# Performance work log

Hardware: AMD Instinct MI355X
Metric: run time of the kernel (lower is better)

The kernel has to match this reference:

```python
import jax, jax.numpy as jnp
import numpy as np

B, T, C, HS = 4, 4096, 1024, 128

def setup_inputs() -> dict:
    key = jax.random.key(0)
    kx, kq, kk, kv = jax.random.split(key, 4)
    x = jax.random.normal(kx, (B, T, C), dtype=jnp.float32)
    # bias-free Linear weights, stored as (in, out) so projection is x @ W
    scale = 1.0 / np.sqrt(C)
    Wq = jax.random.normal(kq, (C, HS), dtype=jnp.float32) * scale
    Wk = jax.random.normal(kk, (C, HS), dtype=jnp.float32) * scale
    Wv = jax.random.normal(kv, (C, HS), dtype=jnp.float32) * scale
    return {"x": x, "Wq": Wq, "Wk": Wk, "Wv": Wv}

def reference(x, Wq, Wk, Wv):
    # x: (B,T,C) -> q,k,v: (B,T,HS)
    q = jnp.einsum('btc,ch->bth', x, Wq)
    k = jnp.einsum('btc,ch->bth', x, Wk)
    v = jnp.einsum('btc,ch->bth', x, Wv)
    hs = k.shape[-1]
    # scaled scores (B,T,T) with causal mask
    wei = jnp.einsum('bth,bsh->bts', q, k) * (hs ** -0.5)
    causal = jnp.tril(jnp.ones((q.shape[1], q.shape[1]), dtype=bool))
    wei = jnp.where(causal, wei, -jnp.inf)
    wei = jax.nn.softmax(wei, axis=-1)
    # dropout p=0.0 -> identity
    out = jnp.einsum('bts,bsh->bth', wei, v)
    return out
```

## Files before the change

### kernel.cpp

```cpp
#include <hip/hip_runtime.h>
#include <hip/hip_bf16.h>

typedef __attribute__((ext_vector_type(8))) short short8;
typedef __attribute__((ext_vector_type(4))) float f32x4;
typedef __attribute__((ext_vector_type(16))) float f32x16;

#define BATCH 4
#define TLEN 4096
#define CDIM 1024
#define HSD 128
#define MROWS (BATCH*TLEN)

#define QSCALE 0.12751744f

__device__ __forceinline__ unsigned short f2bf(float f){
    unsigned u = __builtin_bit_cast(unsigned, f);
    u = (u + 0x7FFFu + ((u >> 16) & 1u)) >> 16;
    return (unsigned short)u;
}
__device__ __forceinline__ unsigned pkbf(float a, float b){
    unsigned ua = (__builtin_bit_cast(unsigned, a) + 0x8000u) >> 16;
    unsigned ub = (__builtin_bit_cast(unsigned, b) + 0x8000u) & 0xFFFF0000u;
    return ua | ub;
}

__global__ void prep_w_k(const float* __restrict__ Wq, const float* __restrict__ Wk,
                         const float* __restrict__ Wv, unsigned short* __restrict__ Wt){
    __shared__ float tile[32][33];
    const int w = blockIdx.z;
    const float* W = (w == 0) ? Wq : ((w == 1) ? Wk : Wv);
    const int c0 = blockIdx.x * 32, h0 = blockIdx.y * 32;
    const int lx = threadIdx.x & 31, ly = threadIdx.x >> 5;
#pragma unroll
    for (int i = 0; i < 4; i++){
        int c = c0 + ly + i * 8;
        tile[ly + i * 8][lx] = W[(size_t)c * HSD + h0 + lx];
    }
    __syncthreads();
#pragma unroll
    for (int i = 0; i < 4; i++){
        int h = h0 + ly + i * 8;
        Wt[((size_t)w * HSD + h) * CDIM + c0 + lx] = f2bf(tile[lx][ly + i * 8]);
    }
}

__device__ __forceinline__ void stage_wb(unsigned short* buf, const unsigned short* g, int tid){
#pragma unroll
    for (int i = 0; i < 3; i++){
        int c = i * 512 + tid;
        int row = c >> 2, kp = c & 3;
        int swz = (row & 3) ^ ((row >> 2) & 3);
        const unsigned short* gp = g + (size_t)row * CDIM + ((kp ^ swz) << 3);
        unsigned short* lp = buf + (c << 3);
        __builtin_amdgcn_global_load_lds((const __attribute__((address_space(1))) void*)gp,
                                         (__attribute__((address_space(3))) void*)lp, 16, 0, 0);
    }
}

__global__ __launch_bounds__(512) void proj_k(const float* __restrict__ x,
                                              const unsigned short* __restrict__ Wt,
                                              unsigned short* __restrict__ Qb,
                                              unsigned short* __restrict__ Kb,
                                              unsigned short* __restrict__ Vt){
    __shared__ unsigned short As[2][64 * 32];
    __shared__ unsigned short Bs[2][384 * 32];

    const int tid = threadIdx.x, lane = tid & 63, wave = tid >> 6;
    const int m = lane & 15, quad = lane >> 4;
    const int wr = wave & 1;
    const int wc = wave >> 1;
    const int rb = blockIdx.x * 64;

    const float* gA = x + (size_t)rb * CDIM;

    const int arow = tid >> 3, ach = tid & 7;
    const int asw = (arow & 3) ^ ((arow >> 2) & 3);
    const float* agp = gA + (size_t)arow * CDIM + ((((ach >> 1) ^ asw) << 3) + (ach & 1) * 4);
    unsigned short* asp0 = &As[0][arow * 32 + (ach << 2)];
    unsigned short* asp1 = &As[1][arow * 32 + (ach << 2)];

    f32x4 acc[6][2];
#pragma unroll
    for (int i = 0; i < 6; i++)
#pragma unroll
        for (int j = 0; j < 2; j++) acc[i][j] = (f32x4)0.f;

    stage_wb(&Bs[0][0], Wt, tid);
    {
        float4 a0 = *(const float4*)(agp);
        ushort4 o;
        o.x = f2bf(a0.x); o.y = f2bf(a0.y); o.z = f2bf(a0.z); o.w = f2bf(a0.w);
        *(ushort4*)asp0 = o;
    }
    __syncthreads();

    int cur = 0;
    for (int kc = 0; kc < CDIM / 32; ++kc){
        float4 a0n;
        if (kc + 1 < CDIM / 32){
            a0n = *(const float4*)(agp + (kc + 1) * 32);
            stage_wb(&Bs[cur ^ 1][0], Wt + (kc + 1) * 32, tid);
            asm volatile("s_waitcnt vmcnt(4)" ::: "memory");
        } else {
            asm volatile("s_waitcnt vmcnt(0)" ::: "memory");
        }
        __builtin_amdgcn_s_barrier();
        __builtin_amdgcn_sched_barrier(0);
        {
            short8 aF[6], bF[2];
#pragma unroll
            for (int i = 0; i < 6; i++){
                int ra = wc * 96 + i * 16 + m;
                int sa = (ra & 3) ^ ((ra >> 2) & 3);
                aF[i] = *(const short8*)&Bs[cur][ra * 32 + ((quad ^ sa) << 3)];
            }
#pragma unroll
            for (int j = 0; j < 2; j++){
                int rn = wr * 32 + j * 16 + m;
                int sb = (rn & 3) ^ ((rn >> 2) & 3);
                bF[j] = *(const short8*)&As[cur][rn * 32 + ((quad ^ sb) << 3)];
            }
#pragma unroll
            for (int i = 0; i < 6; i++)
#pragma unroll
                for (int j = 0; j < 2; j++)
                    acc[i][j] = __builtin_amdgcn_mfma_f32_16x16x32_bf16(aF[i], bF[j], acc[i][j], 0, 0, 0);
        }
        if (kc + 1 < CDIM / 32){
            ushort4 o;
            o.x = f2bf(a0n.x); o.y = f2bf(a0n.y); o.z = f2bf(a0n.z); o.w = f2bf(a0n.w);
            *(ushort4*)((cur == 0) ? asp1 : asp0) = o;
        }
        cur ^= 1;
    }
    __builtin_amdgcn_s_barrier();

    const int b = rb >> 12;
#pragma unroll
    for (int i = 0; i < 6; i++){
        const int hbase = wc * 96 + i * 16;
        const int type = hbase >> 7;
        const int hp = hbase + quad * 4;
#pragma unroll
        for (int j = 0; j < 2; j++){
            const int t = rb + wr * 32 + j * 16 + m;
            if (type == 0){
                ushort4 v;
                v.x = f2bf(acc[i][j][0] * QSCALE); v.y = f2bf(acc[i][j][1] * QSCALE);
                v.z = f2bf(acc[i][j][2] * QSCALE); v.w = f2bf(acc[i][j][3] * QSCALE);
                *(ushort4*)(Qb + (size_t)t * HSD + hp) = v;
            } else if (type == 1){
                ushort4 v;
                v.x = f2bf(acc[i][j][0]); v.y = f2bf(acc[i][j][1]);
                v.z = f2bf(acc[i][j][2]); v.w = f2bf(acc[i][j][3]);
                *(ushort4*)(Kb + (size_t)t * HSD + (hp - 128)) = v;
            } else {
                const int tt = t & (TLEN - 1);
#pragma unroll
                for (int r = 0; r < 4; r++)
                    Vt[((size_t)b * HSD + (hp - 256 + r)) * TLEN + tt] = f2bf(acc[i][j][r]);
            }
        }
    }
}

__device__ __forceinline__ void stage_k_tile(unsigned short* buf, const unsigned short* g,
                                             int tid){
#pragma unroll
    for (int i = 0; i < 2; i++){
        int slot = i * 256 + tid;
        int row = slot >> 4;
        int ch  = slot & 15;
        const unsigned short* gp = g + row * 128 + ((ch ^ (row & 15)) << 3);
        unsigned short* lp = buf + (slot << 3);
        __builtin_amdgcn_global_load_lds((const __attribute__((address_space(1))) void*)gp,
                                         (__attribute__((address_space(3))) void*)lp, 16, 0, 0);
    }
}
__device__ __forceinline__ void stage_v_tile(unsigned short* buf, const unsigned short* g,
                                             int tid){
#pragma unroll
    for (int i = 0; i < 2; i++){
        int slot = i * 256 + tid;
        int row = slot >> 2;
        int ch  = slot & 3;
        const unsigned short* gp = g + (size_t)row * TLEN + ((ch ^ (row & 3)) << 3);
        unsigned short* lp = buf + (slot << 3);
        __builtin_amdgcn_global_load_lds((const __attribute__((address_space(1))) void*)gp,
                                         (__attribute__((address_space(3))) void*)lp, 16, 0, 0);
    }
}

__global__ __launch_bounds__(256, 3) void attn_k(const unsigned short* __restrict__ Qb,
                       const unsigned short* __restrict__ Kb,
                       const unsigned short* __restrict__ Vts,
                       float* __restrict__ Opart, float* __restrict__ lpart, int seglen){
    __shared__ unsigned short Kt[2][32 * 128];
    __shared__ unsigned short Vs[2][128 * 32];

    const int tid = threadIdx.x, lane = tid & 63, wave = tid >> 6;
    const int col = lane & 31, half = lane >> 5;
    const int q0 = ((int)gridDim.x - 1 - (int)blockIdx.x) * 128;
    const int seg = blockIdx.y, b = blockIdx.z;
    const int g0 = seg * seglen;
    if (g0 >= q0 + 128) return;
    const int gend = min(g0 + seglen, q0 + 128);
    const int nT = (gend - g0) >> 5;

    const int q0w = q0 + wave * 32;
    const size_t rowg = (size_t)b * TLEN + q0w;

    const unsigned short* kbase = Kb + (size_t)b * TLEN * HSD;
    const unsigned short* vbase = Vts + (size_t)b * HSD * TLEN;

    short8 aQ[8];
#pragma unroll
    for (int ks = 0; ks < 8; ks++)
        aQ[ks] = *(const short8*)(Qb + (rowg + col) * HSD + ks * 16 + half * 8);

    stage_k_tile(&Kt[0][0], kbase + (size_t)g0 * HSD, tid);
    stage_v_tile(&Vs[0][0], vbase + g0, tid);

    f32x16 accO[4];
#pragma unroll
    for (int i = 0; i < 4; i++) accO[i] = (f32x16)0.f;
    float lp = 0.f;

    asm volatile("s_waitcnt vmcnt(0)" ::: "memory");
#pragma unroll
    for (int ks = 0; ks < 8; ks++){
        f32x4 q_ = __builtin_bit_cast(f32x4, aQ[ks]);
        asm volatile("" : "+v"(q_));
        aQ[ks] = __builtin_bit_cast(short8, q_);
    }

    int cur = 0;
    for (int t = 0; t < nT; ++t){
        const int s0 = g0 + t * 32;
        if (t + 1 < nT){
            stage_k_tile(&Kt[cur ^ 1][0], kbase + (size_t)(s0 + 32) * HSD, tid);
            stage_v_tile(&Vs[cur ^ 1][0], vbase + (s0 + 32), tid);
            asm volatile("s_waitcnt vmcnt(4)" ::: "memory");
        } else {
            asm volatile("s_waitcnt vmcnt(0)" ::: "memory");
        }
        __builtin_amdgcn_s_barrier();
        __builtin_amdgcn_sched_barrier(0);
        if (s0 <= q0w + 31){
            const unsigned short* Ktc = &Kt[cur][0];
            const unsigned short* Vsc = &Vs[cur][0];
            f32x16 S = (f32x16)0.f;
            __builtin_amdgcn_s_setprio(1);
#pragma unroll
            for (int ks = 0; ks < 8; ks++){
                short8 aK = *(const short8*)&Ktc[col * 128 + (((ks * 2 + half) ^ (col & 15)) << 3)];
                S = __builtin_amdgcn_mfma_f32_32x32x16_bf16(aK, aQ[ks], S, 0, 0, 0);
            }
            __builtin_amdgcn_s_setprio(0);
            if (s0 + 31 > q0w){
                int qg = q0w + col;
#pragma unroll
                for (int r = 0; r < 16; r++){
                    int sg = s0 + (r & 3) + 8 * (r >> 2) + 4 * half;
                    if (sg > qg) S[r] = -1e30f;
                }
            }
            float p[16];
#pragma unroll
            for (int r = 0; r < 16; r++) p[r] = exp2f(S[r]);
#pragma unroll
            for (int r = 0; r < 16; r++) lp += p[r];
            short8 aP[2];
            {
                unsigned x1 = pkbf(p[0], p[1]), x2 = pkbf(p[2], p[3]);
                unsigned y1 = pkbf(p[4], p[5]), y2 = pkbf(p[6], p[7]);
                asm volatile("v_permlane32_swap_b32 %0, %1" : "+v"(x1), "+v"(y1));
                asm volatile("v_permlane32_swap_b32 %0, %1" : "+v"(x2), "+v"(y2));
                uint4 u; u.x = x1; u.y = x2; u.z = y1; u.w = y2;
                aP[0] = __builtin_bit_cast(short8, u);
                unsigned z1 = pkbf(p[8], p[9]),  z2 = pkbf(p[10], p[11]);
                unsigned w1 = pkbf(p[12], p[13]), w2 = pkbf(p[14], p[15]);
                asm volatile("v_permlane32_swap_b32 %0, %1" : "+v"(z1), "+v"(w1));
                asm volatile("v_permlane32_swap_b32 %0, %1" : "+v"(z2), "+v"(w2));
                uint4 u2; u2.x = z1; u2.y = z2; u2.z = w1; u2.w = w2;
                aP[1] = __builtin_bit_cast(short8, u2);
            }
            __builtin_amdgcn_s_setprio(1);
#pragma unroll
            for (int ks = 0; ks < 2; ks++){
#pragma unroll
                for (int ht = 0; ht < 4; ht++){
                    short8 bV = *(const short8*)&Vsc[(ht * 32 + col) * 32 +
                            (((ks * 2 + half) ^ (col & 3)) << 3)];
                    accO[ht] = __builtin_amdgcn_mfma_f32_32x32x16_bf16(aP[ks], bV, accO[ht], 0, 0, 0);
                }
            }
            __builtin_amdgcn_s_setprio(0);
        }
        __builtin_amdgcn_sched_barrier(0);
        __builtin_amdgcn_s_barrier();
        cur ^= 1;
    }
    lp += __shfl_xor(lp, 32, 64);
    if (lane < 32)
        lpart[(size_t)seg * MROWS + rowg + col] = lp;
    float* ob = Opart + (size_t)seg * MROWS * HSD;
#pragma unroll
    for (int ht = 0; ht < 4; ht++)
#pragma unroll
        for (int r = 0; r < 16; r++){
            int qrow = (r & 3) + 8 * (r >> 2) + 4 * half;
            ob[(rowg + qrow) * HSD + ht * 32 + col] = accO[ht][r];
        }
}

__global__ void merge_k(const float* __restrict__ Opart, const float* __restrict__ lpart,
                        float* __restrict__ out, int nseg, int seglen){
    int idx = blockIdx.x * 256 + threadIdx.x;
    int row = idx >> 7;
    int t = row & (TLEN - 1);
    int q0 = t & ~127;
    int nsv = min(nseg, (q0 + 127) / seglen + 1);
    float L = 0.f, o = 0.f;
    for (int s = 0; s < nsv; s++){
        L += lpart[(size_t)s * MROWS + row];
        o += Opart[(size_t)s * MROWS * HSD + idx];
    }
    out[idx] = o / L;
}

extern "C" void kernel_launch(void* const* d_in, const int* in_sizes, int n_in,
                              void* d_out, int out_size, void* d_ws, size_t ws_size,
                              hipStream_t stream) {
    const float* x  = (const float*)d_in[0];
    const float* Wq = (const float*)d_in[1];
    const float* Wk = (const float*)d_in[2];
    const float* Wv = (const float*)d_in[3];
    float* out = (float*)d_out;
    char* w = (char*)d_ws;

    unsigned short* Wt = (unsigned short*)w;
    unsigned short* Qb = (unsigned short*)(w + ((size_t)1u  << 20));
    unsigned short* Kb = (unsigned short*)(w + ((size_t)5u  << 20));
    unsigned short* Vt = (unsigned short*)(w + ((size_t)9u  << 20));
    float* lpart       = (float*)(w + ((size_t)13u << 20));
    float* Opart;
    int nseg;
    const size_t segbytes = (size_t)MROWS * HSD * 4;
    if (ws_size >= ((size_t)14u << 20) + 8 * segbytes){
        nseg = 8;  Opart = (float*)(w + ((size_t)14u << 20));
    } else if (ws_size >= ((size_t)14u << 20) + 4 * segbytes){
        nseg = 4;  Opart = (float*)(w + ((size_t)14u << 20));
    } else {
        nseg = 1;  Opart = out;
    }
    const int seglen = TLEN / nseg;

    prep_w_k<<<dim3(CDIM / 32, HSD / 32, 3), 256, 0, stream>>>(Wq, Wk, Wv, Wt);
    proj_k<<<dim3(MROWS / 64), 512, 0, stream>>>(x, Wt, Qb, Kb, Vt);
    attn_k<<<dim3(TLEN / 128, nseg, BATCH), 256, 0, stream>>>(Qb, Kb, Vt, Opart, lpart, seglen);
    merge_k<<<(MROWS * HSD) / 256, 256, 0, stream>>>(Opart, lpart, out, nseg, seglen);
}
```

Measured before the change: 195.2 us.

## Shrink attention blocks to two waves, drop double buffering, allow sixteen segments

The attention kernel now uses 128-thread blocks covering 64 query rows instead of 256 threads and 128 rows. K/V staging becomes single-buffered with a full wait on each tile, and launch bounds rise to five blocks per CU. The host can pick 16 key segments when the workspace allows, with merge indexing adjusted to match. This aims for more blocks, finer causal load balance and higher occupancy, at the cost of losing load/compute overlap within a block, reloading each K/V tile for half as many query rows, and more partial-output traffic in the merge.

```diff
diff --git a/kernel.cpp b/kernel.cpp
--- a/kernel.cpp
+++ b/kernel.cpp
@@ -167,8 +167,8 @@
 __device__ __forceinline__ void stage_k_tile(unsigned short* buf, const unsigned short* g,
                                              int tid){
 #pragma unroll
-    for (int i = 0; i < 2; i++){
-        int slot = i * 256 + tid;
+    for (int i = 0; i < 4; i++){
+        int slot = i * 128 + tid;
         int row = slot >> 4;
         int ch  = slot & 15;
         const unsigned short* gp = g + row * 128 + ((ch ^ (row & 15)) << 3);
@@ -180,8 +180,8 @@
 __device__ __forceinline__ void stage_v_tile(unsigned short* buf, const unsigned short* g,
                                              int tid){
 #pragma unroll
-    for (int i = 0; i < 2; i++){
-        int slot = i * 256 + tid;
+    for (int i = 0; i < 4; i++){
+        int slot = i * 128 + tid;
         int row = slot >> 2;
         int ch  = slot & 3;
         const unsigned short* gp = g + (size_t)row * TLEN + ((ch ^ (row & 3)) << 3);
@@ -191,20 +191,20 @@
     }
 }
 
-__global__ __launch_bounds__(256, 3) void attn_k(const unsigned short* __restrict__ Qb,
+__global__ __launch_bounds__(128, 5) void attn_k(const unsigned short* __restrict__ Qb,
                        const unsigned short* __restrict__ Kb,
                        const unsigned short* __restrict__ Vts,
                        float* __restrict__ Opart, float* __restrict__ lpart, int seglen){
-    __shared__ unsigned short Kt[2][32 * 128];
-    __shared__ unsigned short Vs[2][128 * 32];
+    __shared__ unsigned short Kt[32 * 128];
+    __shared__ unsigned short Vs[128 * 32];
 
     const int tid = threadIdx.x, lane = tid & 63, wave = tid >> 6;
     const int col = lane & 31, half = lane >> 5;
-    const int q0 = ((int)gridDim.x - 1 - (int)blockIdx.x) * 128;
+    const int q0 = ((int)gridDim.x - 1 - (int)blockIdx.x) * 64;
     const int seg = blockIdx.y, b = blockIdx.z;
     const int g0 = seg * seglen;
-    if (g0 >= q0 + 128) return;
-    const int gend = min(g0 + seglen, q0 + 128);
+    if (g0 >= q0 + 64) return;
+    const int gend = min(g0 + seglen, q0 + 64);
     const int nT = (gend - g0) >> 5;
 
     const int q0w = q0 + wave * 32;
@@ -218,42 +218,24 @@
     for (int ks = 0; ks < 8; ks++)
         aQ[ks] = *(const short8*)(Qb + (rowg + col) * HSD + ks * 16 + half * 8);
 
-    stage_k_tile(&Kt[0][0], kbase + (size_t)g0 * HSD, tid);
-    stage_v_tile(&Vs[0][0], vbase + g0, tid);
-
     f32x16 accO[4];
 #pragma unroll
     for (int i = 0; i < 4; i++) accO[i] = (f32x16)0.f;
     float lp = 0.f;
 
-    asm volatile("s_waitcnt vmcnt(0)" ::: "memory");
-#pragma unroll
-    for (int ks = 0; ks < 8; ks++){
-        f32x4 q_ = __builtin_bit_cast(f32x4, aQ[ks]);
-        asm volatile("" : "+v"(q_));
-        aQ[ks] = __builtin_bit_cast(short8, q_);
-    }
-
-    int cur = 0;
     for (int t = 0; t < nT; ++t){
         const int s0 = g0 + t * 32;
-        if (t + 1 < nT){
-            stage_k_tile(&Kt[cur ^ 1][0], kbase + (size_t)(s0 + 32) * HSD, tid);
-            stage_v_tile(&Vs[cur ^ 1][0], vbase + (s0 + 32), tid);
-            asm volatile("s_waitcnt vmcnt(4)" ::: "memory");
-        } else {
-            asm volatile("s_waitcnt vmcnt(0)" ::: "memory");
-        }
+        stage_k_tile(&Kt[0], kbase + (size_t)s0 * HSD, tid);
+        stage_v_tile(&Vs[0], vbase + s0, tid);
+        asm volatile("s_waitcnt vmcnt(0)" ::: "memory");
         __builtin_amdgcn_s_barrier();
         __builtin_amdgcn_sched_barrier(0);
         if (s0 <= q0w + 31){
-            const unsigned short* Ktc = &Kt[cur][0];
-            const unsigned short* Vsc = &Vs[cur][0];
             f32x16 S = (f32x16)0.f;
             __builtin_amdgcn_s_setprio(1);
 #pragma unroll
             for (int ks = 0; ks < 8; ks++){
-                short8 aK = *(const short8*)&Ktc[col * 128 + (((ks * 2 + half) ^ (col & 15)) << 3)];
+                short8 aK = *(const short8*)&Kt[col * 128 + (((ks * 2 + half) ^ (col & 15)) << 3)];
                 S = __builtin_amdgcn_mfma_f32_32x32x16_bf16(aK, aQ[ks], S, 0, 0, 0);
             }
             __builtin_amdgcn_s_setprio(0);
@@ -290,7 +272,7 @@
             for (int ks = 0; ks < 2; ks++){
 #pragma unroll
                 for (int ht = 0; ht < 4; ht++){
-                    short8 bV = *(const short8*)&Vsc[(ht * 32 + col) * 32 +
+                    short8 bV = *(const short8*)&Vs[(ht * 32 + col) * 32 +
                             (((ks * 2 + half) ^ (col & 3)) << 3)];
                     accO[ht] = __builtin_amdgcn_mfma_f32_32x32x16_bf16(aP[ks], bV, accO[ht], 0, 0, 0);
                 }
@@ -299,7 +281,6 @@
         }
         __builtin_amdgcn_sched_barrier(0);
         __builtin_amdgcn_s_barrier();
-        cur ^= 1;
     }
     lp += __shfl_xor(lp, 32, 64);
     if (lane < 32)
@@ -319,8 +300,8 @@
     int idx = blockIdx.x * 256 + threadIdx.x;
     int row = idx >> 7;
     int t = row & (TLEN - 1);
-    int q0 = t & ~127;
-    int nsv = min(nseg, (q0 + 127) / seglen + 1);
+    int q0 = t & ~63;
+    int nsv = min(nseg, (q0 + 63) / seglen + 1);
     float L = 0.f, o = 0.f;
     for (int s = 0; s < nsv; s++){
         L += lpart[(size_t)s * MROWS + row];
@@ -347,7 +328,9 @@
     float* Opart;
     int nseg;
     const size_t segbytes = (size_t)MROWS * HSD * 4;
-    if (ws_size >= ((size_t)14u << 20) + 8 * segbytes){
+    if (ws_size >= ((size_t)14u << 20) + 16 * segbytes){
+        nseg = 16; Opart = (float*)(w + ((size_t)14u << 20));
+    } else if (ws_size >= ((size_t)14u << 20) + 8 * segbytes){
         nseg = 8;  Opart = (float*)(w + ((size_t)14u << 20));
     } else if (ws_size >= ((size_t)14u << 20) + 4 * segbytes){
         nseg = 4;  Opart = (float*)(w + ((size_t)14u << 20));
@@ -358,6 +341,6 @@
 
     prep_w_k<<<dim3(CDIM / 32, HSD / 32, 3), 256, 0, stream>>>(Wq, Wk, Wv, Wt);
     proj_k<<<dim3(MROWS / 64), 512, 0, stream>>>(x, Wt, Qb, Kb, Vt);
-    attn_k<<<dim3(TLEN / 128, nseg, BATCH), 256, 0, stream>>>(Qb, Kb, Vt, Opart, lpart, seglen);
+    attn_k<<<dim3(TLEN / 64, nseg, BATCH), 128, 0, stream>>>(Qb, Kb, Vt, Opart, lpart, seglen);
     merge_k<<<(MROWS * HSD) / 256, 256, 0, stream>>>(Opart, lpart, out, nseg, seglen);
 }
```

Result: slower. 378.6 us (+93.9%).

## Replace split-KV partial buffers with atomic accumulation and finer sequence split

Applied to the files above, without the earlier changes.

The attention kernel now adds its unnormalized partial outputs directly into the zeroed output with atomicAdd, instead of writing per-segment partial buffers. A lighter normalization kernel then only sums the per-segment row sums and divides. The KV sequence is split into a fixed 16 segments for more parallelism. The V tile shared-memory layout is changed to a 64x64 swizzled arrangement that packs two head rows per LDS row. This removes the large partial-output traffic and the merge pass, at the cost of many global atomics, a memset and nondeterministic summation order.

```diff
diff --git a/kernel.cpp b/kernel.cpp
--- a/kernel.cpp
+++ b/kernel.cpp
@@ -182,9 +182,10 @@
 #pragma unroll
     for (int i = 0; i < 2; i++){
         int slot = i * 256 + tid;
-        int row = slot >> 2;
-        int ch  = slot & 3;
-        const unsigned short* gp = g + (size_t)row * TLEN + ((ch ^ (row & 3)) << 3);
+        int row = slot >> 3;
+        int ch  = slot & 7;
+        int lc  = ch ^ (row & 7);
+        const unsigned short* gp = g + (size_t)(2 * row + (lc >> 2)) * TLEN + ((lc & 3) << 3);
         unsigned short* lp = buf + (slot << 3);
         __builtin_amdgcn_global_load_lds((const __attribute__((address_space(1))) void*)gp,
                                          (__attribute__((address_space(3))) void*)lp, 16, 0, 0);
@@ -194,9 +195,9 @@
 __global__ __launch_bounds__(256, 3) void attn_k(const unsigned short* __restrict__ Qb,
                        const unsigned short* __restrict__ Kb,
                        const unsigned short* __restrict__ Vts,
-                       float* __restrict__ Opart, float* __restrict__ lpart, int seglen){
+                       float* __restrict__ out, float* __restrict__ lpart, int seglen){
     __shared__ unsigned short Kt[2][32 * 128];
-    __shared__ unsigned short Vs[2][128 * 32];
+    __shared__ unsigned short Vs[2][64 * 64];
 
     const int tid = threadIdx.x, lane = tid & 63, wave = tid >> 6;
     const int col = lane & 31, half = lane >> 5;
@@ -290,8 +291,10 @@
             for (int ks = 0; ks < 2; ks++){
 #pragma unroll
                 for (int ht = 0; ht < 4; ht++){
-                    short8 bV = *(const short8*)&Vsc[(ht * 32 + col) * 32 +
-                            (((ks * 2 + half) ^ (col & 3)) << 3)];
+                    int h = ht * 32 + col;
+                    int lc = ((h & 1) << 2) + ks * 2 + half;
+                    short8 bV = *(const short8*)&Vsc[(h >> 1) * 64 +
+                            ((lc ^ ((h >> 1) & 7)) << 3)];
                     accO[ht] = __builtin_amdgcn_mfma_f32_32x32x16_bf16(aP[ks], bV, accO[ht], 0, 0, 0);
                 }
             }
@@ -304,29 +307,27 @@
     lp += __shfl_xor(lp, 32, 64);
     if (lane < 32)
         lpart[(size_t)seg * MROWS + rowg + col] = lp;
-    float* ob = Opart + (size_t)seg * MROWS * HSD;
+    float* ob = out;
 #pragma unroll
     for (int ht = 0; ht < 4; ht++)
 #pragma unroll
         for (int r = 0; r < 16; r++){
             int qrow = (r & 3) + 8 * (r >> 2) + 4 * half;
-            ob[(rowg + qrow) * HSD + ht * 32 + col] = accO[ht][r];
-        }
-}
-
-__global__ void merge_k(const float* __restrict__ Opart, const float* __restrict__ lpart,
-                        float* __restrict__ out, int nseg, int seglen){
+            atomicAdd(&ob[(rowg + qrow) * HSD + ht * 32 + col], accO[ht][r]);
+        }
+}
+
+__global__ void norm_k(float* __restrict__ out, const float* __restrict__ lpart,
+                       int nseg, int seglen){
     int idx = blockIdx.x * 256 + threadIdx.x;
     int row = idx >> 7;
     int t = row & (TLEN - 1);
     int q0 = t & ~127;
     int nsv = min(nseg, (q0 + 127) / seglen + 1);
-    float L = 0.f, o = 0.f;
-    for (int s = 0; s < nsv; s++){
+    float L = 0.f;
+    for (int s = 0; s < nsv; s++)
         L += lpart[(size_t)s * MROWS + row];
-        o += Opart[(size_t)s * MROWS * HSD + idx];
-    }
-    out[idx] = o / L;
+    out[idx] = out[idx] / L;
 }
 
 extern "C" void kernel_launch(void* const* d_in, const int* in_sizes, int n_in,
@@ -344,20 +345,12 @@
     unsigned short* Kb = (unsigned short*)(w + ((size_t)5u  << 20));
     unsigned short* Vt = (unsigned short*)(w + ((size_t)9u  << 20));
     float* lpart       = (float*)(w + ((size_t)13u << 20));
-    float* Opart;
-    int nseg;
-    const size_t segbytes = (size_t)MROWS * HSD * 4;
-    if (ws_size >= ((size_t)14u << 20) + 8 * segbytes){
-        nseg = 8;  Opart = (float*)(w + ((size_t)14u << 20));
-    } else if (ws_size >= ((size_t)14u << 20) + 4 * segbytes){
-        nseg = 4;  Opart = (float*)(w + ((size_t)14u << 20));
-    } else {
-        nseg = 1;  Opart = out;
-    }
+    const int nseg = 16;
     const int seglen = TLEN / nseg;
 
+    hipMemsetAsync(out, 0, (size_t)MROWS * HSD * sizeof(float), stream);
     prep_w_k<<<dim3(CDIM / 32, HSD / 32, 3), 256, 0, stream>>>(Wq, Wk, Wv, Wt);
     proj_k<<<dim3(MROWS / 64), 512, 0, stream>>>(x, Wt, Qb, Kb, Vt);
-    attn_k<<<dim3(TLEN / 128, nseg, BATCH), 256, 0, stream>>>(Qb, Kb, Vt, Opart, lpart, seglen);
-    merge_k<<<(MROWS * HSD) / 256, 256, 0, stream>>>(Opart, lpart, out, nseg, seglen);
-}
+    attn_k<<<dim3(TLEN / 128, nseg, BATCH), 256, 0, stream>>>(Qb, Kb, Vt, out, lpart, seglen);
+    norm_k<<<(MROWS * HSD) / 256, 256, 0, stream>>>(out, lpart, nseg, seglen);
+}
```

Result: slower. 224.6 us (+15.1%).
